# Kernel optimization log

Measured on AMD Instinct MI355X. Metric: run time of the kernel, lower is better.

## Reference

```python
import jax, jax.numpy as jnp
import numpy as np

CONF_TH = 0.9
FRACTION = 0.66
IGNORE = 255
LAMBDA = 1.0


def _image_mask(max_prob, lab, num_classes):
    """max_prob: [N] float, lab: [N] int32 pseudo labels. Returns [N] bool mask.

    Faithful to the torch loop: per class c, keep the top int(count_c * FRACTION)
    pixels of that class by confidence, OR any pixel with confidence > CONF_TH.
    Implemented with ONE sort per image + within-class cumulative rank.
    """
    N = max_prob.shape[0]
    mask_prob = max_prob > CONF_TH
    # per-class pixel counts and top-k budget (int() truncates in torch)
    counts = jnp.zeros((num_classes,), jnp.int32).at[lab].add(1)
    k = (counts.astype(jnp.float32) * FRACTION).astype(jnp.int32)
    # sort pixels by confidence descending (stable; no ties with random floats)
    order = jnp.argsort(-max_prob)
    lab_s = lab[order]
    # within-class rank in sorted order: rank 0 = most confident pixel of its class
    onehot = jax.nn.one_hot(lab_s, num_classes, dtype=jnp.int32)  # [N, C]
    rank = jnp.take_along_axis(jnp.cumsum(onehot, axis=0), lab_s[:, None], axis=1)[:, 0] - 1
    sel_s = rank < k[lab_s]
    mask_topk = jnp.zeros((N,), bool).at[order].set(sel_s)
    return mask_prob | mask_topk


def setup_inputs() -> dict:
    key = jax.random.key(0)
    pred = jax.random.normal(key, (8, 19, 512, 1024), dtype=jnp.float32)
    return {"pred": pred}


def reference(pred):
    B, C, H, W = pred.shape
    N = H * W
    # teacher is None -> pseudo labels from pred itself (detached)
    pred_sg = jax.lax.stop_gradient(pred)
    prob = jax.nn.softmax(pred_sg, axis=1)
    max_prob = prob.max(axis=1).reshape(B, N)          # [B, N]
    lab = jnp.argmax(pred_sg, axis=1).astype(jnp.int32).reshape(B, N)  # [B, N]
    mask = jax.vmap(lambda mp, l: _image_mask(mp, l, C))(max_prob, lab)  # [B, N] bool
    pseudo = jnp.where(mask, lab, IGNORE)
    # cross-entropy with ignore_index, mean over kept pixels
    logp = jax.nn.log_softmax(pred, axis=1)            # [B, C, H, W]
    logp = logp.transpose(0, 2, 3, 1).reshape(B, N, C)  # [B, N, C]
    valid = pseudo != IGNORE
    tgt = jnp.where(valid, pseudo, 0)
    nll = -jnp.take_along_axis(logp, tgt[:, :, None], axis=2)[:, :, 0]  # [B, N]
    denom = jnp.maximum(jnp.sum(valid), 1).astype(pred.dtype)
    loss = jnp.sum(nll * valid.astype(pred.dtype)) / denom
    return loss * LAMBDA
```

## Files before the change

kernel.cpp:

```cpp
#include <hip/hip_runtime.h>
#include <stdint.h>

#define BLK 256

constexpr int Bsz = 8, Ccls = 19, Hh = 512, Ww = 1024;
constexpr int Npix = Hh * Ww;
constexpr int TotPix = Bsz * Npix;
constexpr int NGroup = Bsz * Ccls;
constexpr int SUBS = 64;
constexpr int NB1 = 256;
constexpr int NB2 = 4096;
constexpr int KEY_BASE = 122 << 5;

__device__ __forceinline__ int key1_of(uint32_t u) {
  int k = (int)(u >> 18) - KEY_BASE;
  return k < 0 ? 0 : (k > 255 ? 255 : k);
}

__global__ __launch_bounds__(BLK) void k_fused(const float* __restrict__ pred,
                                               float4* __restrict__ mp_out,
                                               uchar4* __restrict__ lab_out,
                                               uint32_t* __restrict__ h1) {
  __shared__ uint32_t hist[Ccls * NB1];
  int t = threadIdx.x;
#pragma unroll
  for (int c = 0; c < Ccls; ++c) hist[c * NB1 + t] = 0;
  __syncthreads();

  int blk = blockIdx.x;
  int b = blk >> 6;
  int s = blk & 63;
  const float* ibase = pred + (size_t)b * Ccls * Npix;
  int n0 = s * 8192;

  for (int j = 0; j < 8; ++j) {
    int n = n0 + j * 1024 + t * 4;
    float4 v[Ccls];
#pragma unroll
    for (int c = 0; c < Ccls; ++c)
      v[c] = *(const float4*)(ibase + (size_t)c * Npix + n);

    float mp[4]; int lc[4];
#pragma unroll
    for (int q = 0; q < 4; ++q) {
      float m = ((const float*)&v[0])[q]; int l = 0;
#pragma unroll
      for (int c = 1; c < Ccls; ++c) {
        float x = ((const float*)&v[c])[q];
        if (x > m) { m = x; l = c; }
      }
      float sum = 0.f;
#pragma unroll
      for (int c = 0; c < Ccls; ++c) sum += __expf(((const float*)&v[c])[q] - m);
      mp[q] = 1.0f / sum;
      lc[q] = l;
      uint32_t u = __float_as_uint(mp[q]);
      atomicAdd(&hist[l * NB1 + key1_of(u)], 1u);
    }
    int p4 = b * (Npix / 4) + n / 4;
    mp_out[p4] = make_float4(mp[0], mp[1], mp[2], mp[3]);
    lab_out[p4] = make_uchar4((uint8_t)lc[0], (uint8_t)lc[1], (uint8_t)lc[2], (uint8_t)lc[3]);
  }

  __syncthreads();
  uint32_t* dst = h1 + (size_t)blk * (Ccls * NB1);
#pragma unroll
  for (int c = 0; c < Ccls; ++c) dst[c * NB1 + t] = hist[c * NB1 + t];
}

__global__ __launch_bounds__(BLK) void k_select1(const uint32_t* __restrict__ h1,
                                                 int* __restrict__ selhi,
                                                 int* __restrict__ rem) {
  int g = blockIdx.x;
  int b = g / Ccls, c = g % Ccls;
  int t = threadIdx.x;
  int bin = NB1 - 1 - t;
  uint32_t cnt = 0;
  for (int s = 0; s < SUBS; ++s)
    cnt += h1[(size_t)(b * SUBS + s) * (Ccls * NB1) + c * NB1 + bin];
  __shared__ uint32_t sc[BLK];
  sc[t] = cnt;
  __syncthreads();
  for (int ofs = 1; ofs < BLK; ofs <<= 1) {
    uint32_t vv = (t >= ofs) ? sc[t - ofs] : 0u;
    __syncthreads();
    sc[t] += vv;
    __syncthreads();
  }
  uint32_t incl = sc[t];
  uint32_t excl = incl - cnt;
  uint32_t total = sc[BLK - 1];
  int k = (int)((float)total * 0.66f);
  if (t == 0 && k == 0) { selhi[g] = -1; rem[g] = 0; }
  if (k > 0 && (int)excl < k && k <= (int)incl) {
    selhi[g] = bin;
    rem[g] = k - (int)excl;
  }
}

__global__ __launch_bounds__(BLK) void k_hist2(const float4* __restrict__ mp,
                                               const uchar4* __restrict__ lab,
                                               const int* __restrict__ selhi,
                                               uint32_t* __restrict__ hist2) {
  int p4 = blockIdx.x * BLK + threadIdx.x;
  int b = p4 >> 17;
  float4 m = mp[p4];
  uchar4 l = lab[p4];
  const float* mf = (const float*)&m;
  const uint8_t* lf = (const uint8_t*)&l;
#pragma unroll
  for (int q = 0; q < 4; ++q) {
    uint32_t u = __float_as_uint(mf[q]);
    int g = b * Ccls + (int)lf[q];
    if (key1_of(u) == selhi[g])
      atomicAdd(&hist2[g * NB2 + (int)((u >> 6) & 0xFFFu)], 1u);
  }
}

__global__ __launch_bounds__(BLK) void k_select2(const uint32_t* __restrict__ hist2,
                                                 const int* __restrict__ selhi,
                                                 const int* __restrict__ rem,
                                                 uint32_t* __restrict__ thresh) {
  int g = blockIdx.x;
  int t = threadIdx.x;
  int sh = selhi[g];
  if (sh < 0) { if (t == 0) thresh[g] = 0x7F800000u; return; }
  const uint32_t* h = hist2 + g * NB2;
  uint32_t loc[16]; uint32_t psum = 0;
  int hi = NB2 - 1 - t * 16;
#pragma unroll
  for (int i = 0; i < 16; ++i) { loc[i] = h[hi - i]; psum += loc[i]; }
  __shared__ uint32_t sc[BLK];
  sc[t] = psum;
  __syncthreads();
  for (int ofs = 1; ofs < BLK; ofs <<= 1) {
    uint32_t vv = (t >= ofs) ? sc[t - ofs] : 0u;
    __syncthreads();
    sc[t] += vv;
    __syncthreads();
  }
  uint32_t incl = sc[t];
  int k = rem[g];
  uint32_t excl = incl - psum;
  if (k > 0 && (int)excl < k && k <= (int)incl) {
    uint32_t cum = excl;
#pragma unroll
    for (int i = 0; i < 16; ++i) {
      if ((uint32_t)k <= cum + loc[i]) {
        thresh[g] = ((uint32_t)(sh + KEY_BASE) << 18) | ((uint32_t)(hi - i) << 6);
        break;
      }
      cum += loc[i];
    }
  }
}

__global__ __launch_bounds__(BLK) void k_loss(const float4* __restrict__ mp_arr,
                                              const uchar4* __restrict__ lab,
                                              const uint32_t* __restrict__ thresh,
                                              float* __restrict__ gsum,
                                              uint32_t* __restrict__ gcnt) {
  int p4 = blockIdx.x * BLK + threadIdx.x;
  int b = p4 >> 17;
  float4 m = mp_arr[p4];
  uchar4 l = lab[p4];
  const float* mf = (const float*)&m;
  const uint8_t* lf = (const uint8_t*)&l;
  float vs = 0.f; uint32_t vc = 0u;
#pragma unroll
  for (int q = 0; q < 4; ++q) {
    float mp = mf[q];
    int g = b * Ccls + (int)lf[q];
    uint32_t u = __float_as_uint(mp);
    bool sel = (mp > 0.9f) || (u >= thresh[g]);
    if (sel) { vs += -logf(mp); vc += 1u; }
  }
#pragma unroll
  for (int o = 32; o > 0; o >>= 1) {
    vs += __shfl_down(vs, o, 64);
    vc += __shfl_down(vc, o, 64);
  }
  __shared__ float ssum[BLK / 64];
  __shared__ uint32_t scnt[BLK / 64];
  int wave = threadIdx.x >> 6;
  int lane = threadIdx.x & 63;
  if (lane == 0) { ssum[wave] = vs; scnt[wave] = vc; }
  __syncthreads();
  if (threadIdx.x == 0) {
    float ts = 0.f; uint32_t tc = 0u;
#pragma unroll
    for (int w = 0; w < BLK / 64; ++w) { ts += ssum[w]; tc += scnt[w]; }
    atomicAdd(gsum, ts);
    atomicAdd(gcnt, tc);
  }
}

__global__ void k_final(const float* __restrict__ gsum,
                        const uint32_t* __restrict__ gcnt,
                        float* __restrict__ out) {
  uint32_t c = *gcnt;
  float d = (float)(c > 0u ? c : 1u);
  out[0] = *gsum / d;
}

extern "C" void kernel_launch(void* const* d_in, const int* in_sizes, int n_in,
                              void* d_out, int out_size, void* d_ws, size_t ws_size,
                              hipStream_t stream) {
  const float* pred = (const float*)d_in[0];
  char* ws = (char*)d_ws;
  size_t off = 0;
  auto carve = [&](size_t bytes) -> void* {
    void* p = ws + off;
    off = (off + bytes + 255) & ~(size_t)255;
    return p;
  };
  float*    mp    = (float*)carve((size_t)TotPix * 4);
  uint8_t*  lab   = (uint8_t*)carve((size_t)TotPix);
  uint32_t* h1    = (uint32_t*)carve((size_t)Bsz * SUBS * Ccls * NB1 * 4);
  int*      selhi = (int*)carve((size_t)NGroup * 4);
  int*      rem   = (int*)carve((size_t)NGroup * 4);
  uint32_t* thr   = (uint32_t*)carve((size_t)NGroup * 4);
  size_t zero_off = off;
  uint32_t* hist2 = (uint32_t*)carve((size_t)NGroup * NB2 * 4);
  float*    gsum  = (float*)carve(4);
  uint32_t* gcnt  = (uint32_t*)carve(4);

  hipMemsetAsync(ws + zero_off, 0, off - zero_off, stream);

  int nblk4 = TotPix / (BLK * 4);
  k_fused  <<<Bsz * SUBS, BLK, 0, stream>>>(pred, (float4*)mp, (uchar4*)lab, h1);
  k_select1<<<NGroup,     BLK, 0, stream>>>(h1, selhi, rem);
  k_hist2  <<<nblk4,      BLK, 0, stream>>>((const float4*)mp, (const uchar4*)lab, selhi, hist2);
  k_select2<<<NGroup,     BLK, 0, stream>>>(hist2, selhi, rem, thr);
  k_loss   <<<nblk4,      BLK, 0, stream>>>((const float4*)mp, (const uchar4*)lab, thr, gsum, gcnt);
  k_final  <<<1, 1, 0, stream>>>(gsum, gcnt, (float*)d_out);
}
```

Baseline: 496.5 us.

## Use online softmax with chunked class loads, double fused grid, fold final into loss

The fused first pass now computes max, argmax and the softmax denominator online over class chunks of six. This replaces holding all 19 float4 values in registers, cutting register pressure so more waves can stay resident. The grid doubles to 128 sub-blocks per image (half the pixels each), giving more blocks to spread across CUs, though it also doubles the per-block histogram traffic that k_select1 has to reduce. The separate k_final launch is removed: the last block of k_loss, found with an atomic ticket counter, writes the final mean. The online update does roughly twice the exp calls per element.

```diff
diff --git a/kernel.cpp b/kernel.cpp
--- a/kernel.cpp
+++ b/kernel.cpp
@@ -7,7 +7,7 @@
 constexpr int Npix = Hh * Ww;
 constexpr int TotPix = Bsz * Npix;
 constexpr int NGroup = Bsz * Ccls;
-constexpr int SUBS = 64;
+constexpr int SUBS = 128;
 constexpr int NB1 = 256;
 constexpr int NB2 = 4096;
 constexpr int KEY_BASE = 122 << 5;
@@ -28,36 +28,44 @@
   __syncthreads();
 
   int blk = blockIdx.x;
-  int b = blk >> 6;
-  int s = blk & 63;
+  int b = blk >> 7;
+  int s = blk & 127;
   const float* ibase = pred + (size_t)b * Ccls * Npix;
-  int n0 = s * 8192;
-
-  for (int j = 0; j < 8; ++j) {
+  int n0 = s * 4096;
+
+  for (int j = 0; j < 4; ++j) {
     int n = n0 + j * 1024 + t * 4;
-    float4 v[Ccls];
-#pragma unroll
-    for (int c = 0; c < Ccls; ++c)
-      v[c] = *(const float4*)(ibase + (size_t)c * Npix + n);
-
-    float mp[4]; int lc[4];
+    float4 v0 = *(const float4*)(ibase + n);
+    float m[4] = {v0.x, v0.y, v0.z, v0.w};
+    float sm[4] = {1.f, 1.f, 1.f, 1.f};
+    int lc[4] = {0, 0, 0, 0};
+    for (int cb = 1; cb < Ccls; cb += 6) {
+      float4 vv[6];
+#pragma unroll
+      for (int i = 0; i < 6; ++i)
+        vv[i] = *(const float4*)(ibase + (size_t)(cb + i) * Npix + n);
+#pragma unroll
+      for (int i = 0; i < 6; ++i) {
+        int c = cb + i;
+        const float* vf = (const float*)&vv[i];
+#pragma unroll
+        for (int q = 0; q < 4; ++q) {
+          float x = vf[q];
+          bool gt = x > m[q];
+          float mn = gt ? x : m[q];
+          sm[q] = sm[q] * __expf(m[q] - mn) + __expf(x - mn);
+          m[q] = mn;
+          lc[q] = gt ? c : lc[q];
+        }
+      }
+    }
+    float mp[4];
 #pragma unroll
     for (int q = 0; q < 4; ++q) {
-      float m = ((const float*)&v[0])[q]; int l = 0;
-#pragma unroll
-      for (int c = 1; c < Ccls; ++c) {
-        float x = ((const float*)&v[c])[q];
-        if (x > m) { m = x; l = c; }
-      }
-      float sum = 0.f;
-#pragma unroll
-      for (int c = 0; c < Ccls; ++c) sum += __expf(((const float*)&v[c])[q] - m);
-      mp[q] = 1.0f / sum;
-      lc[q] = l;
-      uint32_t u = __float_as_uint(mp[q]);
-      atomicAdd(&hist[l * NB1 + key1_of(u)], 1u);
-    }
-    int p4 = b * (Npix / 4) + n / 4;
+      mp[q] = 1.0f / sm[q];
+      atomicAdd(&hist[lc[q] * NB1 + key1_of(__float_as_uint(mp[q]))], 1u);
+    }
+    int p4 = b * (Npix / 4) + (n >> 2);
     mp_out[p4] = make_float4(mp[0], mp[1], mp[2], mp[3]);
     lab_out[p4] = make_uchar4((uint8_t)lc[0], (uint8_t)lc[1], (uint8_t)lc[2], (uint8_t)lc[3]);
   }
@@ -159,7 +167,9 @@
                                               const uchar4* __restrict__ lab,
                                               const uint32_t* __restrict__ thresh,
                                               float* __restrict__ gsum,
-                                              uint32_t* __restrict__ gcnt) {
+                                              uint32_t* __restrict__ gcnt,
+                                              uint32_t* __restrict__ ticket,
+                                              float* __restrict__ out) {
   int p4 = blockIdx.x * BLK + threadIdx.x;
   int b = p4 >> 17;
   float4 m = mp_arr[p4];
@@ -192,15 +202,14 @@
     for (int w = 0; w < BLK / 64; ++w) { ts += ssum[w]; tc += scnt[w]; }
     atomicAdd(gsum, ts);
     atomicAdd(gcnt, tc);
-  }
-}
-
-__global__ void k_final(const float* __restrict__ gsum,
-                        const uint32_t* __restrict__ gcnt,
-                        float* __restrict__ out) {
-  uint32_t c = *gcnt;
-  float d = (float)(c > 0u ? c : 1u);
-  out[0] = *gsum / d;
+    __threadfence();
+    uint32_t done = atomicAdd(ticket, 1u);
+    if (done == gridDim.x - 1) {
+      float fs = atomicAdd(gsum, 0.0f);
+      uint32_t fc = atomicAdd(gcnt, 0u);
+      out[0] = fs / (float)(fc > 0u ? fc : 1u);
+    }
+  }
 }
 
 extern "C" void kernel_launch(void* const* d_in, const int* in_sizes, int n_in,
@@ -224,6 +233,7 @@
   uint32_t* hist2 = (uint32_t*)carve((size_t)NGroup * NB2 * 4);
   float*    gsum  = (float*)carve(4);
   uint32_t* gcnt  = (uint32_t*)carve(4);
+  uint32_t* tick  = (uint32_t*)carve(4);
 
   hipMemsetAsync(ws + zero_off, 0, off - zero_off, stream);
 
@@ -232,6 +242,6 @@
   k_select1<<<NGroup,     BLK, 0, stream>>>(h1, selhi, rem);
   k_hist2  <<<nblk4,      BLK, 0, stream>>>((const float4*)mp, (const uchar4*)lab, selhi, hist2);
   k_select2<<<NGroup,     BLK, 0, stream>>>(hist2, selhi, rem, thr);
-  k_loss   <<<nblk4,      BLK, 0, stream>>>((const float4*)mp, (const uchar4*)lab, thr, gsum, gcnt);
-  k_final  <<<1, 1, 0, stream>>>(gsum, gcnt, (float*)d_out);
-}
+  k_loss   <<<nblk4,      BLK, 0, stream>>>((const float4*)mp, (const uchar4*)lab, thr,
+                                            gsum, gcnt, tick, (float*)d_out);
+}
```

New measurement: 536.4 us. +8.0%, slower.

## Replace two-pass radix select with single fine global histogram and fused finalize

Applied to the files above, without the earlier changes.

Drops the coarse 256-bin shared histogram plus a second refinement pass and uses one 10240-bin per-(image,class) global histogram, built with global atomics in the fused softmax kernel. The threshold is then selected in one pass, which removes the select1 and hist2 kernels and the extra read of mp/lab. The final division is folded into the loss kernel through a last-block ticket. The trade-off is that all histogram increments now go to contended global atomics. Thresholds also lose precision, since bins are 12-bit truncated keys rather than 6-bit, so selection can differ from exact top-k near bin boundaries.

```diff
diff --git a/kernel.cpp b/kernel.cpp
--- a/kernel.cpp
+++ b/kernel.cpp
@@ -7,34 +7,26 @@
 constexpr int Npix = Hh * Ww;
 constexpr int TotPix = Bsz * Npix;
 constexpr int NGroup = Bsz * Ccls;
-constexpr int SUBS = 64;
-constexpr int NB1 = 256;
-constexpr int NB2 = 4096;
-constexpr int KEY_BASE = 122 << 5;
+constexpr int NB = 10240;
+constexpr int KEY_BASE = 122 << 11;
 
-__device__ __forceinline__ int key1_of(uint32_t u) {
-  int k = (int)(u >> 18) - KEY_BASE;
-  return k < 0 ? 0 : (k > 255 ? 255 : k);
+__device__ __forceinline__ int key_of(uint32_t u) {
+  int k = (int)(u >> 12) - KEY_BASE;
+  return k < 0 ? 0 : (k > NB - 1 ? NB - 1 : k);
 }
 
 __global__ __launch_bounds__(BLK) void k_fused(const float* __restrict__ pred,
                                                float4* __restrict__ mp_out,
                                                uchar4* __restrict__ lab_out,
-                                               uint32_t* __restrict__ h1) {
-  __shared__ uint32_t hist[Ccls * NB1];
+                                               uint32_t* __restrict__ hist) {
   int t = threadIdx.x;
-#pragma unroll
-  for (int c = 0; c < Ccls; ++c) hist[c * NB1 + t] = 0;
-  __syncthreads();
+  int blk = blockIdx.x;
+  int b = blk >> 7;
+  int s = blk & 127;
+  const float* ibase = pred + (size_t)b * Ccls * Npix;
 
-  int blk = blockIdx.x;
-  int b = blk >> 6;
-  int s = blk & 63;
-  const float* ibase = pred + (size_t)b * Ccls * Npix;
-  int n0 = s * 8192;
-
-  for (int j = 0; j < 8; ++j) {
-    int n = n0 + j * 1024 + t * 4;
+  for (int j = 0; j < 4; ++j) {
+    int n = s * 4096 + j * 1024 + t * 4;
     float4 v[Ccls];
 #pragma unroll
     for (int c = 0; c < Ccls; ++c)
@@ -54,82 +46,23 @@
       for (int c = 0; c < Ccls; ++c) sum += __expf(((const float*)&v[c])[q] - m);
       mp[q] = 1.0f / sum;
       lc[q] = l;
-      uint32_t u = __float_as_uint(mp[q]);
-      atomicAdd(&hist[l * NB1 + key1_of(u)], 1u);
+      atomicAdd(&hist[(size_t)(b * Ccls + l) * NB + key_of(__float_as_uint(mp[q]))], 1u);
     }
-    int p4 = b * (Npix / 4) + n / 4;
+    int p4 = b * (Npix / 4) + (n >> 2);
     mp_out[p4] = make_float4(mp[0], mp[1], mp[2], mp[3]);
     lab_out[p4] = make_uchar4((uint8_t)lc[0], (uint8_t)lc[1], (uint8_t)lc[2], (uint8_t)lc[3]);
   }
-
-  __syncthreads();
-  uint32_t* dst = h1 + (size_t)blk * (Ccls * NB1);
-#pragma unroll
-  for (int c = 0; c < Ccls; ++c) dst[c * NB1 + t] = hist[c * NB1 + t];
 }
 
-__global__ __launch_bounds__(BLK) void k_select1(const uint32_t* __restrict__ h1,
-                                                 int* __restrict__ selhi,
-                                                 int* __restrict__ rem) {
-  int g = blockIdx.x;
-  int b = g / Ccls, c = g % Ccls;
-  int t = threadIdx.x;
-  int bin = NB1 - 1 - t;
-  uint32_t cnt = 0;
-  for (int s = 0; s < SUBS; ++s)
-    cnt += h1[(size_t)(b * SUBS + s) * (Ccls * NB1) + c * NB1 + bin];
-  __shared__ uint32_t sc[BLK];
-  sc[t] = cnt;
-  __syncthreads();
-  for (int ofs = 1; ofs < BLK; ofs <<= 1) {
-    uint32_t vv = (t >= ofs) ? sc[t - ofs] : 0u;
-    __syncthreads();
-    sc[t] += vv;
-    __syncthreads();
-  }
-  uint32_t incl = sc[t];
-  uint32_t excl = incl - cnt;
-  uint32_t total = sc[BLK - 1];
-  int k = (int)((float)total * 0.66f);
-  if (t == 0 && k == 0) { selhi[g] = -1; rem[g] = 0; }
-  if (k > 0 && (int)excl < k && k <= (int)incl) {
-    selhi[g] = bin;
-    rem[g] = k - (int)excl;
-  }
-}
-
-__global__ __launch_bounds__(BLK) void k_hist2(const float4* __restrict__ mp,
-                                               const uchar4* __restrict__ lab,
-                                               const int* __restrict__ selhi,
-                                               uint32_t* __restrict__ hist2) {
-  int p4 = blockIdx.x * BLK + threadIdx.x;
-  int b = p4 >> 17;
-  float4 m = mp[p4];
-  uchar4 l = lab[p4];
-  const float* mf = (const float*)&m;
-  const uint8_t* lf = (const uint8_t*)&l;
-#pragma unroll
-  for (int q = 0; q < 4; ++q) {
-    uint32_t u = __float_as_uint(mf[q]);
-    int g = b * Ccls + (int)lf[q];
-    if (key1_of(u) == selhi[g])
-      atomicAdd(&hist2[g * NB2 + (int)((u >> 6) & 0xFFFu)], 1u);
-  }
-}
-
-__global__ __launch_bounds__(BLK) void k_select2(const uint32_t* __restrict__ hist2,
-                                                 const int* __restrict__ selhi,
-                                                 const int* __restrict__ rem,
-                                                 uint32_t* __restrict__ thresh) {
+__global__ __launch_bounds__(BLK) void k_select(const uint32_t* __restrict__ hist,
+                                                uint32_t* __restrict__ thresh) {
   int g = blockIdx.x;
   int t = threadIdx.x;
-  int sh = selhi[g];
-  if (sh < 0) { if (t == 0) thresh[g] = 0x7F800000u; return; }
-  const uint32_t* h = hist2 + g * NB2;
-  uint32_t loc[16]; uint32_t psum = 0;
-  int hi = NB2 - 1 - t * 16;
+  const uint32_t* h = hist + (size_t)g * NB;
+  uint32_t loc[40]; uint32_t psum = 0;
+  int hi = NB - 1 - t * 40;
 #pragma unroll
-  for (int i = 0; i < 16; ++i) { loc[i] = h[hi - i]; psum += loc[i]; }
+  for (int i = 0; i < 40; ++i) { loc[i] = h[hi - i]; psum += loc[i]; }
   __shared__ uint32_t sc[BLK];
   sc[t] = psum;
   __syncthreads();
@@ -140,14 +73,16 @@
     __syncthreads();
   }
   uint32_t incl = sc[t];
-  int k = rem[g];
   uint32_t excl = incl - psum;
+  uint32_t total = sc[BLK - 1];
+  int k = (int)((float)total * 0.66f);
+  if (t == 0 && k == 0) thresh[g] = 0x7F800000u;
   if (k > 0 && (int)excl < k && k <= (int)incl) {
     uint32_t cum = excl;
 #pragma unroll
-    for (int i = 0; i < 16; ++i) {
+    for (int i = 0; i < 40; ++i) {
       if ((uint32_t)k <= cum + loc[i]) {
-        thresh[g] = ((uint32_t)(sh + KEY_BASE) << 18) | ((uint32_t)(hi - i) << 6);
+        thresh[g] = (uint32_t)(hi - i + KEY_BASE) << 12;
         break;
       }
       cum += loc[i];
@@ -159,7 +94,9 @@
                                               const uchar4* __restrict__ lab,
                                               const uint32_t* __restrict__ thresh,
                                               float* __restrict__ gsum,
-                                              uint32_t* __restrict__ gcnt) {
+                                              uint32_t* __restrict__ gcnt,
+                                              uint32_t* __restrict__ ticket,
+                                              float* __restrict__ out) {
   int p4 = blockIdx.x * BLK + threadIdx.x;
   int b = p4 >> 17;
   float4 m = mp_arr[p4];
@@ -192,15 +129,14 @@
     for (int w = 0; w < BLK / 64; ++w) { ts += ssum[w]; tc += scnt[w]; }
     atomicAdd(gsum, ts);
     atomicAdd(gcnt, tc);
+    __threadfence();
+    uint32_t done = atomicAdd(ticket, 1u);
+    if (done == gridDim.x - 1) {
+      float fs = atomicAdd(gsum, 0.0f);
+      uint32_t fc = atomicAdd(gcnt, 0u);
+      out[0] = fs / (float)(fc > 0u ? fc : 1u);
+    }
   }
-}
-
-__global__ void k_final(const float* __restrict__ gsum,
-                        const uint32_t* __restrict__ gcnt,
-                        float* __restrict__ out) {
-  uint32_t c = *gcnt;
-  float d = (float)(c > 0u ? c : 1u);
-  out[0] = *gsum / d;
 }
 
 extern "C" void kernel_launch(void* const* d_in, const int* in_sizes, int n_in,
@@ -216,22 +152,18 @@
   };
   float*    mp    = (float*)carve((size_t)TotPix * 4);
   uint8_t*  lab   = (uint8_t*)carve((size_t)TotPix);
-  uint32_t* h1    = (uint32_t*)carve((size_t)Bsz * SUBS * Ccls * NB1 * 4);
-  int*      selhi = (int*)carve((size_t)NGroup * 4);
-  int*      rem   = (int*)carve((size_t)NGroup * 4);
   uint32_t* thr   = (uint32_t*)carve((size_t)NGroup * 4);
   size_t zero_off = off;
-  uint32_t* hist2 = (uint32_t*)carve((size_t)NGroup * NB2 * 4);
+  uint32_t* hist  = (uint32_t*)carve((size_t)NGroup * NB * 4);
   float*    gsum  = (float*)carve(4);
   uint32_t* gcnt  = (uint32_t*)carve(4);
+  uint32_t* tick  = (uint32_t*)carve(4);
 
   hipMemsetAsync(ws + zero_off, 0, off - zero_off, stream);
 
   int nblk4 = TotPix / (BLK * 4);
-  k_fused  <<<Bsz * SUBS, BLK, 0, stream>>>(pred, (float4*)mp, (uchar4*)lab, h1);
-  k_select1<<<NGroup,     BLK, 0, stream>>>(h1, selhi, rem);
-  k_hist2  <<<nblk4,      BLK, 0, stream>>>((const float4*)mp, (const uchar4*)lab, selhi, hist2);
-  k_select2<<<NGroup,     BLK, 0, stream>>>(hist2, selhi, rem, thr);
-  k_loss   <<<nblk4,      BLK, 0, stream>>>((const float4*)mp, (const uchar4*)lab, thr, gsum, gcnt);
-  k_final  <<<1, 1, 0, stream>>>(gsum, gcnt, (float*)d_out);
+  k_fused <<<Bsz * 128, BLK, 0, stream>>>(pred, (float4*)mp, (uchar4*)lab, hist);
+  k_select<<<NGroup,    BLK, 0, stream>>>(hist, thr);
+  k_loss  <<<nblk4,     BLK, 0, stream>>>((const float4*)mp, (const uchar4*)lab, thr,
+                                          gsum, gcnt, tick, (float*)d_out);
 }
```

Result: slower. 615.5 us (+24.0%).
